# Kernel tuning notes

Measured on AMD Instinct MI355X. Metric: run time of the kernel, lower is better.

## Reference

```python
import jax, jax.numpy as jnp
import numpy as np

N_HEADS = 16

def setup_inputs() -> dict:
    key = jax.random.key(0)
    ks = jax.random.split(key, 5)
    b, t, k = 2, 2048, 1024
    x = jax.random.normal(ks[0], (b, t, k), dtype=jnp.float32)
    Wq = jax.random.normal(ks[1], (k, k), dtype=jnp.float32) * 0.02
    Wk = jax.random.normal(ks[2], (k, k), dtype=jnp.float32) * 0.02
    Wv = jax.random.normal(ks[3], (k, k), dtype=jnp.float32) * 0.02
    Wo = jax.random.normal(ks[4], (k, k), dtype=jnp.float32) * 0.02
    return {"x": x, "Wq": Wq, "Wk": Wk, "Wv": Wv, "Wo": Wo}

def reference(x, Wq, Wk, Wv, Wo):
    b, t, k = x.shape
    h = N_HEADS
    hs = k // h
    # torch nn.Linear(k, k, bias=False): y = x @ W.T
    Q = (x @ Wq.T).reshape(b, t, h, hs).transpose(0, 2, 1, 3)  # [b,h,t,hs]
    K = (x @ Wk.T).reshape(b, t, h, hs).transpose(0, 2, 1, 3)
    V = (x @ Wv.T).reshape(b, t, h, hs).transpose(0, 2, 1, 3)
    # NOTE: original scales by 1/sqrt(k) (full model dim), not 1/sqrt(hs)
    scores = jnp.einsum('bhqd,bhkd->bhqk', Q, K) / jnp.sqrt(jnp.float32(k))
    causal = jnp.tril(jnp.ones((t, t), dtype=bool))  # [t,t]
    scores = jnp.where(causal[None, None], scores, jnp.float32(-jnp.inf))
    P = jax.nn.softmax(scores, axis=-1)  # [b,h,t,t]
    O = jnp.einsum('bhqk,bhkd->bhqd', P, V)  # [b,h,t,hs]
    O = O.transpose(0, 2, 1, 3).reshape(b, t, k)
    return O @ Wo.T
```

## Files before the change

### kernel.cpp

```cpp
#include <hip/hip_runtime.h>
#include <hip/hip_bf16.h>

typedef __attribute__((ext_vector_type(8))) short bf16x8;
typedef __attribute__((ext_vector_type(4))) float f32x4;
typedef unsigned short u16;
typedef unsigned int u32;

#define MFMA16(a, b, c) __builtin_amdgcn_mfma_f32_16x16x32_bf16((a), (b), (c), 0, 0, 0)

__device__ __forceinline__ void gld16(const void* g, void* l) {
  __builtin_amdgcn_global_load_lds((const __attribute__((address_space(1))) u32*)g,
                                   (__attribute__((address_space(3))) u32*)l, 16, 0, 0);
}

__device__ __forceinline__ u16 f2bf(float f) {
  u32 x = __float_as_uint(f);
  x += 0x7fffu + ((x >> 16) & 1u);
  return (u16)(x >> 16);
}
__device__ __forceinline__ u32 pk2(float lo, float hi) {
  return (u32)f2bf(lo) | ((u32)f2bf(hi) << 16);
}
__device__ __forceinline__ u32 cvtpk(float lo, float hi) {
  u32 r;
  asm("v_cvt_pk_bf16_f32 %0, %1, %2" : "=v"(r) : "v"(lo), "v"(hi));
  return r;
}
__device__ __forceinline__ bf16x8 ldfrag(const u16* lds, int row, int kbyte) {
  return *(const bf16x8*)&lds[row * 64 + ((kbyte ^ ((row & 7) << 4)) >> 1)];
}

__global__ __launch_bounds__(256) void cvt_bf16(const float* __restrict__ s, u16* __restrict__ d,
                                                int n4) {
  int i = blockIdx.x * 256 + threadIdx.x;
  if (i < n4) {
    float4 f = ((const float4*)s)[i];
    uint2 o;
    o.x = pk2(f.x, f.y);
    o.y = pk2(f.z, f.w);
    ((uint2*)d)[i] = o;
  }
}

__global__ __launch_bounds__(256) void cvt_w4(const float* __restrict__ w0,
                                              const float* __restrict__ w1,
                                              const float* __restrict__ w2,
                                              const float* __restrict__ w3,
                                              u16* __restrict__ d012, u16* __restrict__ d3) {
  const int y = blockIdx.y;
  const float* s = (y == 0) ? w0 : (y == 1) ? w1 : (y == 2) ? w2 : w3;
  u16* d = (y == 3) ? d3 : d012 + (size_t)y * 1024 * 1024;
  int i = blockIdx.x * 256 + threadIdx.x;
  float4 f = ((const float4*)s)[i];
  uint2 o;
  o.x = pk2(f.x, f.y);
  o.y = pk2(f.z, f.w);
  ((uint2*)d)[i] = o;
}

template <int MODE, bool BBF, int BM>
__global__ __launch_bounds__(256) void gemm2(const u16* __restrict__ Ab,
                                             const float* __restrict__ W0,
                                             const float* __restrict__ W1,
                                             const float* __restrict__ W2,
                                             const u16* __restrict__ Bb, u16* __restrict__ Cq,
                                             u16* __restrict__ Ck, u16* __restrict__ Cvt,
                                             float* __restrict__ Cf) {
  constexpr int MI = BM / 32;
  __shared__ u16 Alds[BM * 64];
  __shared__ u16 Blds[128 * 64];
  const int tid = threadIdx.x, wid = tid >> 6, lane = tid & 63;
  const int lg = lane >> 4, lr = lane & 15;
  const int wr = wid >> 1, wc = wid & 1;
  const int bm = blockIdx.y, bn = blockIdx.x;
  const int ng = bn * 128;

  const float* Bf = nullptr;
  const u16* Bbr = nullptr;
  if constexpr (BBF) {
    Bbr = Bb + (size_t)ng * 1024;
  } else {
    if constexpr (MODE == 0)
      Bf = (ng < 1024 ? W0 : (ng < 2048 ? W1 : W2)) + (size_t)(ng & 1023) * 1024;
    else
      Bf = W0 + (size_t)ng * 1024;
  }

  f32x4 acc[MI][4];
#pragma unroll
  for (int i = 0; i < MI; ++i)
#pragma unroll
    for (int j = 0; j < 4; ++j) acc[i][j] = {0.f, 0.f, 0.f, 0.f};

  const u16* Ag0 = Ab + (size_t)(bm * BM) * 1024;
  const int srow8 = lane >> 3, schunk = lane & 7;
  const int brow = tid >> 1, bhalf = tid & 1;

  for (int kt = 0; kt < 16; ++kt) {
    __syncthreads();
#pragma unroll
    for (int c = 0; c < BM / 32; ++c) {
      int rb = (c * 4 + wid) * 8;
      int row = rb + srow8;
      int ch = schunk ^ srow8;
      gld16(Ag0 + (size_t)row * 1024 + kt * 64 + ch * 8, (void*)&Alds[rb * 64]);
    }
    if constexpr (BBF) {
#pragma unroll
      for (int c = 0; c < 4; ++c) {
        int rb = (c * 4 + wid) * 8;
        int row = rb + srow8;
        int ch = schunk ^ srow8;
        gld16(Bbr + (size_t)row * 1024 + kt * 64 + ch * 8, (void*)&Blds[rb * 64]);
      }
    } else {
      const float* s = Bf + (size_t)brow * 1024 + kt * 64 + bhalf * 32;
#pragma unroll
      for (int q = 0; q < 4; ++q) {
        float4 f0 = ((const float4*)s)[2 * q];
        float4 f1 = ((const float4*)s)[2 * q + 1];
        uint4 w;
        w.x = pk2(f0.x, f0.y);
        w.y = pk2(f0.z, f0.w);
        w.z = pk2(f1.x, f1.y);
        w.w = pk2(f1.z, f1.w);
        int ch = (bhalf * 4 + q) ^ (brow & 7);
        *(uint4*)&Blds[brow * 64 + ch * 8] = w;
      }
    }
    __syncthreads();

#pragma unroll
    for (int ks = 0; ks < 2; ++ks) {
      bf16x8 af[MI], bfr[4];
#pragma unroll
      for (int mi = 0; mi < MI; ++mi)
        af[mi] = ldfrag(Alds, wr * (BM / 2) + mi * 16 + lr, ks * 64 + lg * 16);
#pragma unroll
      for (int ni = 0; ni < 4; ++ni) bfr[ni] = ldfrag(Blds, wc * 64 + ni * 16 + lr, ks * 64 + lg * 16);
#pragma unroll
      for (int mi = 0; mi < MI; ++mi)
#pragma unroll
        for (int ni = 0; ni < 4; ++ni) acc[mi][ni] = MFMA16(af[mi], bfr[ni], acc[mi][ni]);
    }
  }

  if constexpr (MODE == 1) {
#pragma unroll
    for (int mi = 0; mi < MI; ++mi)
#pragma unroll
      for (int r = 0; r < 4; ++r) {
        int m = bm * BM + wr * (BM / 2) + mi * 16 + lg * 4 + r;
#pragma unroll
        for (int ni = 0; ni < 4; ++ni)
          Cf[(size_t)m * 1024 + ng + wc * 64 + ni * 16 + lr] = acc[mi][ni][r];
      }
  } else if (ng < 2048) {
    u16* C = (ng < 1024) ? Cq : Ck;
    const float qs = (ng < 1024) ? 0.0450842200f : 1.0f;
    const int nb = ng & 1023;
#pragma unroll
    for (int mi = 0; mi < MI; ++mi)
#pragma unroll
      for (int r = 0; r < 4; ++r) {
        int m = bm * BM + wr * (BM / 2) + mi * 16 + lg * 4 + r;
#pragma unroll
        for (int ni = 0; ni < 4; ++ni)
          C[(size_t)m * 1024 + nb + wc * 64 + ni * 16 + lr] = f2bf(acc[mi][ni][r] * qs);
      }
  } else {
    const int bnum = (bm * BM) >> 11;
    const int nvb = (ng - 2048) + wc * 64;
#pragma unroll
    for (int mi = 0; mi < MI; ++mi) {
      int tb = ((bm * BM) & 2047) + wr * (BM / 2) + mi * 16 + lg * 4;
#pragma unroll
      for (int ni = 0; ni < 4; ++ni) {
        int nv = nvb + ni * 16 + lr;
        ushort4 st;
        st.x = f2bf(acc[mi][ni][0]);
        st.y = f2bf(acc[mi][ni][1]);
        st.z = f2bf(acc[mi][ni][2]);
        st.w = f2bf(acc[mi][ni][3]);
        *(ushort4*)&Cvt[((size_t)(bnum << 10) + nv) * 2048 + tb] = st;
      }
    }
  }
}

__global__ __launch_bounds__(256, 4) void flash6(const u16* __restrict__ Qb,
                                                 const u16* __restrict__ Kb,
                                                 const u16* __restrict__ Vt,
                                                 u16* __restrict__ Ob) {
  __shared__ u16 Klds[2][64 * 64];
  __shared__ u16 Vlds[2][64 * 64];
  __shared__ u16 Plds[4][16 * 64];
  const int tid = threadIdx.x, wid = tid >> 6, lane = tid & 63;
  const int lg = lane >> 4, lr = lane & 15;
  const int bid = blockIdx.x;
  const int xcd = bid & 7;
  const int slot = bid >> 3;
  const int cp = slot & 31;
  const int g = slot >> 5;
  const int hb = xcd * 4 + g;
  const int hh = hb & 15, bb = hb >> 4;
  const int m0 = (cp + ((g >> 1) << 3)) & 31;
  const int base = (m0 & 1) ? (m0 >> 1) : (31 - (m0 >> 1));
  const int jq = (g & 1) ? (31 - base) : base;
  const int q0 = jq * 64;
  const size_t baseqk = ((size_t)bb * 2048) * 1024 + hh * 64;
  const u16* Vth = Vt + ((size_t)(bb * 1024 + hh * 64)) * 2048;
  const int srow8 = lane >> 3, schunk = lane & 7;

  bf16x8 qf[2];
  {
    const u16* qp = Qb + baseqk + (size_t)(q0 + wid * 16 + lr) * 1024 + lg * 8;
    qf[0] = *(const bf16x8*)qp;
    qf[1] = *(const bf16x8*)(qp + 32);
  }
  f32x4 acc[4];
#pragma unroll
  for (int dt = 0; dt < 4; ++dt) acc[dt] = {0.f, 0.f, 0.f, 0.f};
  float l_r = 0.f;
  const int qrow = q0 + wid * 16 + lr;

  auto stage = [&](int buf, int kv0) {
#pragma unroll
    for (int c2 = 0; c2 < 2; ++c2) {
      int rb = (c2 * 4 + wid) * 8;
      int row = rb + srow8;
      int ch = schunk ^ srow8;
      gld16(Kb + baseqk + (size_t)(kv0 + row) * 1024 + ch * 8, (void*)&Klds[buf][rb * 64]);
      gld16(Vth + (size_t)row * 2048 + kv0 + ch * 8, (void*)&Vlds[buf][rb * 64]);
    }
  };

  const int ntiles = jq + 1;
  stage(0, 0);
  __syncthreads();

  u16* Pw = &Plds[wid][0];
  const int pswz = (lr & 7) << 3;

  for (int t = 0; t < ntiles; ++t) {
    const int cur = t & 1;
    if (t + 1 < ntiles) stage(cur ^ 1, (t + 1) * 64);
    const int kv0 = t * 64;
    const u16* Kl = &Klds[cur][0];
    const u16* Vl = &Vlds[cur][0];

    f32x4 s[4];
#pragma unroll
    for (int ni = 0; ni < 4; ++ni) s[ni] = {0.f, 0.f, 0.f, 0.f};
    __builtin_amdgcn_s_setprio(1);
#pragma unroll
    for (int ks = 0; ks < 2; ++ks) {
#pragma unroll
      for (int ni = 0; ni < 4; ++ni) {
        bf16x8 kb = ldfrag(Kl, ni * 16 + lr, ks * 64 + lg * 16);
        s[ni] = MFMA16(kb, qf[ks], s[ni]);
      }
    }
    __builtin_amdgcn_s_setprio(0);

    float p[4][4];
    float rs = 0.f;
    if (t == jq) {
#pragma unroll
      for (int ni = 0; ni < 4; ++ni)
#pragma unroll
        for (int r = 0; r < 4; ++r) {
          float v = s[ni][r];
          if (kv0 + ni * 16 + lg * 4 + r > qrow) v = -1e30f;
          v = exp2f(v);
          p[ni][r] = v;
          rs += v;
        }
    } else {
#pragma unroll
      for (int ni = 0; ni < 4; ++ni)
#pragma unroll
        for (int r = 0; r < 4; ++r) {
          float v = exp2f(s[ni][r]);
          p[ni][r] = v;
          rs += v;
        }
    }
    l_r += rs;

#pragma unroll
    for (int ni = 0; ni < 4; ++ni) {
#pragma unroll
      for (int h = 0; h < 2; ++h) {
        u32 w = cvtpk(p[ni][2 * h], p[ni][2 * h + 1]);
        int col = (ni * 16 + lg * 4 + 2 * h) ^ pswz;
        *(u32*)&Pw[lr * 64 + col] = w;
      }
    }
    bf16x8 pb0 = *(const bf16x8*)&Pw[lr * 64 + ((lg * 8) ^ pswz)];
    bf16x8 pb1 = *(const bf16x8*)&Pw[lr * 64 + ((32 + lg * 8) ^ pswz)];
    __builtin_amdgcn_s_setprio(1);
#pragma unroll
    for (int dt = 0; dt < 4; ++dt) {
      bf16x8 a0 = ldfrag(Vl, dt * 16 + lr, lg * 16);
      bf16x8 a1 = ldfrag(Vl, dt * 16 + lr, 64 + lg * 16);
      acc[dt] = MFMA16(a0, pb0, acc[dt]);
      acc[dt] = MFMA16(a1, pb1, acc[dt]);
    }
    __builtin_amdgcn_s_setprio(0);
    __syncthreads();
  }

  l_r += __shfl_xor(l_r, 16);
  l_r += __shfl_xor(l_r, 32);

  {
    float inv = 1.f / l_r;
    u16* orow = Ob + baseqk + (size_t)qrow * 1024 + lg * 4;
#pragma unroll
    for (int dt = 0; dt < 4; ++dt) {
      ushort4 st;
      st.x = f2bf(acc[dt][0] * inv);
      st.y = f2bf(acc[dt][1] * inv);
      st.z = f2bf(acc[dt][2] * inv);
      st.w = f2bf(acc[dt][3] * inv);
      *(ushort4*)&orow[dt * 16] = st;
    }
  }
}

extern "C" void kernel_launch(void* const* d_in, const int* in_sizes, int n_in, void* d_out,
                              int out_size, void* d_ws, size_t ws_size, hipStream_t stream) {
  const float* x = (const float*)d_in[0];
  const float* Wq = (const float*)d_in[1];
  const float* Wk = (const float*)d_in[2];
  const float* Wv = (const float*)d_in[3];
  const float* Wo = (const float*)d_in[4];
  float* out = (float*)d_out;

  u16* xb = (u16*)d_ws;
  u16* Qb = xb + (size_t)4096 * 1024;
  u16* Kb = Qb + (size_t)4096 * 1024;
  u16* Vt = Kb + (size_t)4096 * 1024;
  u16* Ob = Qb;
  u16* Wb = Vt + (size_t)4096 * 1024;
  u16* Wob = Wb + (size_t)3072 * 1024;

  const bool full = ws_size >= ((size_t)40 << 20);

  cvt_bf16<<<4096, 256, 0, stream>>>(x, xb, 4096 * 1024 / 4);
  if (full) {
    cvt_w4<<<dim3(1024, 4), 256, 0, stream>>>(Wq, Wk, Wv, Wo, Wb, Wob);
    gemm2<0, true, 128><<<dim3(24, 32), 256, 0, stream>>>(xb, nullptr, nullptr, nullptr, Wb, Qb,
                                                          Kb, Vt, nullptr);
    flash6<<<1024, 256, 0, stream>>>(Qb, Kb, Vt, Ob);
    gemm2<1, true, 64><<<dim3(8, 64), 256, 0, stream>>>(Ob, nullptr, nullptr, nullptr, Wob,
                                                        nullptr, nullptr, nullptr, out);
  } else {
    gemm2<0, false, 128><<<dim3(24, 32), 256, 0, stream>>>(xb, Wq, Wk, Wv, nullptr, Qb, Kb, Vt,
                                                           nullptr);
    flash6<<<1024, 256, 0, stream>>>(Qb, Kb, Vt, Ob);
    gemm2<1, false, 64><<<dim3(8, 64), 256, 0, stream>>>(Ob, Wo, nullptr, nullptr, nullptr,
                                                         nullptr, nullptr, nullptr, out);
  }
}
```

Before: 116.2 us.

## Split long causal attention rows across two kernels with partial accumulators

The flash attention kernel now caps every query block at 16 KV tiles. Query blocks past index 16 write unnormalised bf16 partial accumulators and row sums to workspace. A second kernel with 512 blocks reloads those partials and processes the remaining KV tiles before normalising, which splits the longest causal rows across two launches to even out load. In exchange it adds an extra launch, partial round-trips through global memory with bf16 rounding of the accumulators, and a serial dependency. It also reuses the xb buffer as scratch.

```diff
diff --git a/kernel.cpp b/kernel.cpp
--- a/kernel.cpp
+++ b/kernel.cpp
@@ -188,10 +188,11 @@
   }
 }
 
-__global__ __launch_bounds__(256, 4) void flash6(const u16* __restrict__ Qb,
+__global__ __launch_bounds__(256, 4) void flashA(const u16* __restrict__ Qb,
                                                  const u16* __restrict__ Kb,
                                                  const u16* __restrict__ Vt,
-                                                 u16* __restrict__ Ob) {
+                                                 u16* __restrict__ Ob, u16* __restrict__ accP,
+                                                 float* __restrict__ lP) {
   __shared__ u16 Klds[2][64 * 64];
   __shared__ u16 Vlds[2][64 * 64];
   __shared__ u16 Plds[4][16 * 64];
@@ -200,13 +201,14 @@
   const int bid = blockIdx.x;
   const int xcd = bid & 7;
   const int slot = bid >> 3;
-  const int cp = slot & 31;
-  const int g = slot >> 5;
+  const int cp = slot & 31, g = slot >> 5;
   const int hb = xcd * 4 + g;
   const int hh = hb & 15, bb = hb >> 4;
   const int m0 = (cp + ((g >> 1) << 3)) & 31;
-  const int base = (m0 & 1) ? (m0 >> 1) : (31 - (m0 >> 1));
-  const int jq = (g & 1) ? (31 - base) : base;
+  const int basej = (m0 & 1) ? (m0 >> 1) : (31 - (m0 >> 1));
+  const int jq = (g & 1) ? (31 - basej) : basej;
+  const bool split = jq >= 16;
+  const int t1 = split ? 16 : jq + 1;
   const int q0 = jq * 64;
   const size_t baseqk = ((size_t)bb * 2048) * 1024 + hh * 64;
   const u16* Vth = Vt + ((size_t)(bb * 1024 + hh * 64)) * 2048;
@@ -235,16 +237,15 @@
     }
   };
 
-  const int ntiles = jq + 1;
   stage(0, 0);
   __syncthreads();
 
   u16* Pw = &Plds[wid][0];
   const int pswz = (lr & 7) << 3;
 
-  for (int t = 0; t < ntiles; ++t) {
+  for (int t = 0; t < t1; ++t) {
     const int cur = t & 1;
-    if (t + 1 < ntiles) stage(cur ^ 1, (t + 1) * 64);
+    if (t + 1 < t1) stage(cur ^ 1, (t + 1) * 64);
     const int kv0 = t * 64;
     const u16* Kl = &Klds[cur][0];
     const u16* Vl = &Vlds[cur][0];
@@ -265,7 +266,7 @@
 
     float p[4][4];
     float rs = 0.f;
-    if (t == jq) {
+    if (!split && t == jq) {
 #pragma unroll
       for (int ni = 0; ni < 4; ++ni)
 #pragma unroll
@@ -311,8 +312,175 @@
     __syncthreads();
   }
 
+  if (split) {
+    const int pidx = hb * 16 + (jq - 16);
+    u16* pp = accP + ((size_t)(pidx * 64 + wid * 16 + lr)) * 64 + lg * 4;
+#pragma unroll
+    for (int dt = 0; dt < 4; ++dt) {
+      ushort4 st;
+      st.x = f2bf(acc[dt][0]);
+      st.y = f2bf(acc[dt][1]);
+      st.z = f2bf(acc[dt][2]);
+      st.w = f2bf(acc[dt][3]);
+      *(ushort4*)&pp[dt * 16] = st;
+    }
+    l_r += __shfl_xor(l_r, 16);
+    l_r += __shfl_xor(l_r, 32);
+    if (lg == 0) lP[pidx * 64 + wid * 16 + lr] = l_r;
+  } else {
+    l_r += __shfl_xor(l_r, 16);
+    l_r += __shfl_xor(l_r, 32);
+    float inv = 1.f / l_r;
+    u16* orow = Ob + baseqk + (size_t)qrow * 1024 + lg * 4;
+#pragma unroll
+    for (int dt = 0; dt < 4; ++dt) {
+      ushort4 st;
+      st.x = f2bf(acc[dt][0] * inv);
+      st.y = f2bf(acc[dt][1] * inv);
+      st.z = f2bf(acc[dt][2] * inv);
+      st.w = f2bf(acc[dt][3] * inv);
+      *(ushort4*)&orow[dt * 16] = st;
+    }
+  }
+}
+
+__global__ __launch_bounds__(256, 4) void flashB(const u16* __restrict__ Qb,
+                                                 const u16* __restrict__ Kb,
+                                                 const u16* __restrict__ Vt,
+                                                 u16* __restrict__ Ob,
+                                                 const u16* __restrict__ accP,
+                                                 const float* __restrict__ lP) {
+  __shared__ u16 Klds[2][64 * 64];
+  __shared__ u16 Vlds[2][64 * 64];
+  __shared__ u16 Plds[4][16 * 64];
+  const int tid = threadIdx.x, wid = tid >> 6, lane = tid & 63;
+  const int lg = lane >> 4, lr = lane & 15;
+  const int bid = blockIdx.x;
+  const int xcd = bid & 7;
+  const int slot = bid >> 3;
+  const int cp = slot & 15, g = slot >> 4;
+  const int hb = xcd * 4 + g;
+  const int hh = hb & 15, bb = hb >> 4;
+  const int m0 = (cp + ((g >> 1) << 3)) & 15;
+  const int basej = (m0 & 1) ? (m0 >> 1) : (15 - (m0 >> 1));
+  const int jq = 16 + ((g & 1) ? (15 - basej) : basej);
+  const int pidx = hb * 16 + (jq - 16);
+  const int q0 = jq * 64;
+  const size_t baseqk = ((size_t)bb * 2048) * 1024 + hh * 64;
+  const u16* Vth = Vt + ((size_t)(bb * 1024 + hh * 64)) * 2048;
+  const int srow8 = lane >> 3, schunk = lane & 7;
+
+  bf16x8 qf[2];
+  {
+    const u16* qp = Qb + baseqk + (size_t)(q0 + wid * 16 + lr) * 1024 + lg * 8;
+    qf[0] = *(const bf16x8*)qp;
+    qf[1] = *(const bf16x8*)(qp + 32);
+  }
+  const int qrow = q0 + wid * 16 + lr;
+
+  auto stage = [&](int buf, int kv0) {
+#pragma unroll
+    for (int c2 = 0; c2 < 2; ++c2) {
+      int rb = (c2 * 4 + wid) * 8;
+      int row = rb + srow8;
+      int ch = schunk ^ srow8;
+      gld16(Kb + baseqk + (size_t)(kv0 + row) * 1024 + ch * 8, (void*)&Klds[buf][rb * 64]);
+      gld16(Vth + (size_t)row * 2048 + kv0 + ch * 8, (void*)&Vlds[buf][rb * 64]);
+    }
+  };
+
+  stage(0, 16 * 64);
+
+  f32x4 acc[4];
+  {
+    const u16* pp = accP + ((size_t)(pidx * 64 + wid * 16 + lr)) * 64 + lg * 4;
+#pragma unroll
+    for (int dt = 0; dt < 4; ++dt) {
+      ushort4 pv = *(const ushort4*)&pp[dt * 16];
+      acc[dt][0] = __uint_as_float((u32)pv.x << 16);
+      acc[dt][1] = __uint_as_float((u32)pv.y << 16);
+      acc[dt][2] = __uint_as_float((u32)pv.z << 16);
+      acc[dt][3] = __uint_as_float((u32)pv.w << 16);
+    }
+  }
+  float l_r = 0.f;
+  __syncthreads();
+
+  u16* Pw = &Plds[wid][0];
+  const int pswz = (lr & 7) << 3;
+
+  for (int t = 16; t <= jq; ++t) {
+    const int cur = t & 1;
+    if (t < jq) stage(cur ^ 1, (t + 1) * 64);
+    const int kv0 = t * 64;
+    const u16* Kl = &Klds[cur][0];
+    const u16* Vl = &Vlds[cur][0];
+
+    f32x4 s[4];
+#pragma unroll
+    for (int ni = 0; ni < 4; ++ni) s[ni] = {0.f, 0.f, 0.f, 0.f};
+    __builtin_amdgcn_s_setprio(1);
+#pragma unroll
+    for (int ks = 0; ks < 2; ++ks) {
+#pragma unroll
+      for (int ni = 0; ni < 4; ++ni) {
+        bf16x8 kb = ldfrag(Kl, ni * 16 + lr, ks * 64 + lg * 16);
+        s[ni] = MFMA16(kb, qf[ks], s[ni]);
+      }
+    }
+    __builtin_amdgcn_s_setprio(0);
+
+    float p[4][4];
+    float rs = 0.f;
+    if (t == jq) {
+#pragma unroll
+      for (int ni = 0; ni < 4; ++ni)
+#pragma unroll
+        for (int r = 0; r < 4; ++r) {
+          float v = s[ni][r];
+          if (kv0 + ni * 16 + lg * 4 + r > qrow) v = -1e30f;
+          v = exp2f(v);
+          p[ni][r] = v;
+          rs += v;
+        }
+    } else {
+#pragma unroll
+      for (int ni = 0; ni < 4; ++ni)
+#pragma unroll
+        for (int r = 0; r < 4; ++r) {
+          float v = exp2f(s[ni][r]);
+          p[ni][r] = v;
+          rs += v;
+        }
+    }
+    l_r += rs;
+
+#pragma unroll
+    for (int ni = 0; ni < 4; ++ni) {
+#pragma unroll
+      for (int h = 0; h < 2; ++h) {
+        u32 w = cvtpk(p[ni][2 * h], p[ni][2 * h + 1]);
+        int col = (ni * 16 + lg * 4 + 2 * h) ^ pswz;
+        *(u32*)&Pw[lr * 64 + col] = w;
+      }
+    }
+    bf16x8 pb0 = *(const bf16x8*)&Pw[lr * 64 + ((lg * 8) ^ pswz)];
+    bf16x8 pb1 = *(const bf16x8*)&Pw[lr * 64 + ((32 + lg * 8) ^ pswz)];
+    __builtin_amdgcn_s_setprio(1);
+#pragma unroll
+    for (int dt = 0; dt < 4; ++dt) {
+      bf16x8 a0 = ldfrag(Vl, dt * 16 + lr, lg * 16);
+      bf16x8 a1 = ldfrag(Vl, dt * 16 + lr, 64 + lg * 16);
+      acc[dt] = MFMA16(a0, pb0, acc[dt]);
+      acc[dt] = MFMA16(a1, pb1, acc[dt]);
+    }
+    __builtin_amdgcn_s_setprio(0);
+    __syncthreads();
+  }
+
   l_r += __shfl_xor(l_r, 16);
   l_r += __shfl_xor(l_r, 32);
+  l_r += lP[pidx * 64 + wid * 16 + lr];
 
   {
     float inv = 1.f / l_r;
@@ -345,6 +513,8 @@
   u16* Ob = Qb;
   u16* Wb = Vt + (size_t)4096 * 1024;
   u16* Wob = Wb + (size_t)3072 * 1024;
+  u16* accP = xb;
+  float* lP = (float*)(xb + (size_t)512 * 64 * 64);
 
   const bool full = ws_size >= ((size_t)40 << 20);
 
@@ -353,13 +523,15 @@
     cvt_w4<<<dim3(1024, 4), 256, 0, stream>>>(Wq, Wk, Wv, Wo, Wb, Wob);
     gemm2<0, true, 128><<<dim3(24, 32), 256, 0, stream>>>(xb, nullptr, nullptr, nullptr, Wb, Qb,
                                                           Kb, Vt, nullptr);
-    flash6<<<1024, 256, 0, stream>>>(Qb, Kb, Vt, Ob);
+    flashA<<<1024, 256, 0, stream>>>(Qb, Kb, Vt, Ob, accP, lP);
+    flashB<<<512, 256, 0, stream>>>(Qb, Kb, Vt, Ob, accP, lP);
     gemm2<1, true, 64><<<dim3(8, 64), 256, 0, stream>>>(Ob, nullptr, nullptr, nullptr, Wob,
                                                         nullptr, nullptr, nullptr, out);
   } else {
     gemm2<0, false, 128><<<dim3(24, 32), 256, 0, stream>>>(xb, Wq, Wk, Wv, nullptr, Qb, Kb, Vt,
                                                            nullptr);
-    flash6<<<1024, 256, 0, stream>>>(Qb, Kb, Vt, Ob);
+    flashA<<<1024, 256, 0, stream>>>(Qb, Kb, Vt, Ob, accP, lP);
+    flashB<<<512, 256, 0, stream>>>(Qb, Kb, Vt, Ob, accP, lP);
     gemm2<1, false, 64><<<dim3(8, 64), 256, 0, stream>>>(Ob, Wo, nullptr, nullptr, nullptr,
                                                          nullptr, nullptr, nullptr, out);
   }
```

New measurement: 127.7 us. 1.1x slower.

## Split long causal query tiles across KV halves with a combine kernel

Applied to the files above, without the earlier changes.

Query tiles in the upper half of the causal range are split into two KV-range halves, processed by separate blocks that write unnormalized bf16 partial accumulators and row sums. A new combine kernel adds the partials and normalizes into the output. This balances per-block work to about 16 KV tiles and raises the block count so the causal tail is shorter. It adds a kernel launch, extra global memory traffic for partials, and bf16 rounding of partial accumulators.

```diff
diff --git a/kernel.cpp b/kernel.cpp
--- a/kernel.cpp
+++ b/kernel.cpp
@@ -188,10 +188,11 @@
   }
 }
 
-__global__ __launch_bounds__(256, 4) void flash6(const u16* __restrict__ Qb,
+__global__ __launch_bounds__(256, 4) void flashC(const u16* __restrict__ Qb,
                                                  const u16* __restrict__ Kb,
                                                  const u16* __restrict__ Vt,
-                                                 u16* __restrict__ Ob) {
+                                                 u16* __restrict__ Ob, u16* __restrict__ accP,
+                                                 float* __restrict__ lP) {
   __shared__ u16 Klds[2][64 * 64];
   __shared__ u16 Vlds[2][64 * 64];
   __shared__ u16 Plds[4][16 * 64];
@@ -200,14 +201,25 @@
   const int bid = blockIdx.x;
   const int xcd = bid & 7;
   const int slot = bid >> 3;
-  const int cp = slot & 31;
-  const int g = slot >> 5;
+  int g, jq;
+  bool typeY;
+  if (slot < 64) {
+    g = slot >> 4;
+    jq = 16 + (slot & 15);
+    typeY = false;
+  } else {
+    int idx = slot - 64;
+    int len = 16 - (idx >> 3);
+    int j = idx & 7;
+    g = j & 3;
+    typeY = (j >> 2) != 0;
+    jq = typeY ? (15 + len) : (len - 1);
+  }
   const int hb = xcd * 4 + g;
   const int hh = hb & 15, bb = hb >> 4;
-  const int m0 = (cp + ((g >> 1) << 3)) & 31;
-  const int base = (m0 & 1) ? (m0 >> 1) : (31 - (m0 >> 1));
-  const int jq = (g & 1) ? (31 - base) : base;
   const int q0 = jq * 64;
+  const int t0 = typeY ? 16 : 0;
+  const int t1 = (!typeY && jq >= 16) ? 16 : (jq + 1);
   const size_t baseqk = ((size_t)bb * 2048) * 1024 + hh * 64;
   const u16* Vth = Vt + ((size_t)(bb * 1024 + hh * 64)) * 2048;
   const int srow8 = lane >> 3, schunk = lane & 7;
@@ -235,16 +247,15 @@
     }
   };
 
-  const int ntiles = jq + 1;
-  stage(0, 0);
+  stage(0, t0 * 64);
   __syncthreads();
 
   u16* Pw = &Plds[wid][0];
   const int pswz = (lr & 7) << 3;
 
-  for (int t = 0; t < ntiles; ++t) {
+  for (int t = t0; t < t1; ++t) {
     const int cur = t & 1;
-    if (t + 1 < ntiles) stage(cur ^ 1, (t + 1) * 64);
+    if (t + 1 < t1) stage(cur ^ 1, (t + 1) * 64);
     const int kv0 = t * 64;
     const u16* Kl = &Klds[cur][0];
     const u16* Vl = &Vlds[cur][0];
@@ -311,10 +322,9 @@
     __syncthreads();
   }
 
-  l_r += __shfl_xor(l_r, 16);
-  l_r += __shfl_xor(l_r, 32);
-
-  {
+  if (!typeY && jq < 16) {
+    l_r += __shfl_xor(l_r, 16);
+    l_r += __shfl_xor(l_r, 32);
     float inv = 1.f / l_r;
     u16* orow = Ob + baseqk + (size_t)qrow * 1024 + lg * 4;
 #pragma unroll
@@ -326,7 +336,47 @@
       st.w = f2bf(acc[dt][3] * inv);
       *(ushort4*)&orow[dt * 16] = st;
     }
-  }
+  } else {
+    const int p = (typeY ? 512 : 0) + hb * 16 + (jq - 16);
+    u16* pp = accP + (size_t)p * 4096 + (size_t)(wid * 16 + lr) * 64 + lg * 4;
+#pragma unroll
+    for (int dt = 0; dt < 4; ++dt) {
+      ushort4 st;
+      st.x = f2bf(acc[dt][0]);
+      st.y = f2bf(acc[dt][1]);
+      st.z = f2bf(acc[dt][2]);
+      st.w = f2bf(acc[dt][3]);
+      *(ushort4*)&pp[dt * 16] = st;
+    }
+    l_r += __shfl_xor(l_r, 16);
+    l_r += __shfl_xor(l_r, 32);
+    if (lg == 0) lP[p * 64 + wid * 16 + lr] = l_r;
+  }
+}
+
+__global__ __launch_bounds__(256) void fcomb(const u16* __restrict__ accP,
+                                             const float* __restrict__ lP,
+                                             u16* __restrict__ Ob) {
+  const int pid = blockIdx.x, tid = threadIdx.x;
+  const int hb = pid >> 4, jq = 16 + (pid & 15);
+  const int bb = hb >> 4, hh = hb & 15;
+  const int row = tid >> 2, dseg = (tid & 3) << 4;
+  const u16* a0 = accP + (size_t)pid * 4096 + row * 64 + dseg;
+  const u16* a1 = accP + (size_t)(pid + 512) * 4096 + row * 64 + dseg;
+  float inv = 1.f / (lP[pid * 64 + row] + lP[(pid + 512) * 64 + row]);
+  u16 b0[16], b1[16], ov[16];
+  *(uint4*)&b0[0] = ((const uint4*)a0)[0];
+  *(uint4*)&b0[8] = ((const uint4*)a0)[1];
+  *(uint4*)&b1[0] = ((const uint4*)a1)[0];
+  *(uint4*)&b1[8] = ((const uint4*)a1)[1];
+#pragma unroll
+  for (int i = 0; i < 16; ++i) {
+    float f = __uint_as_float((u32)b0[i] << 16) + __uint_as_float((u32)b1[i] << 16);
+    ov[i] = f2bf(f * inv);
+  }
+  u16* od = Ob + (size_t)bb * 2048 * 1024 + (size_t)(jq * 64 + row) * 1024 + hh * 64 + dseg;
+  ((uint4*)od)[0] = *(uint4*)&ov[0];
+  ((uint4*)od)[1] = *(uint4*)&ov[8];
 }
 
 extern "C" void kernel_launch(void* const* d_in, const int* in_sizes, int n_in, void* d_out,
@@ -345,21 +395,25 @@
   u16* Ob = Qb;
   u16* Wb = Vt + (size_t)4096 * 1024;
   u16* Wob = Wb + (size_t)3072 * 1024;
+  u16* accP = xb;
 
   const bool full = ws_size >= ((size_t)40 << 20);
+  float* lP = full ? (float*)Wb : (float*)(Vt + (size_t)4096 * 1024);
 
   cvt_bf16<<<4096, 256, 0, stream>>>(x, xb, 4096 * 1024 / 4);
   if (full) {
     cvt_w4<<<dim3(1024, 4), 256, 0, stream>>>(Wq, Wk, Wv, Wo, Wb, Wob);
     gemm2<0, true, 128><<<dim3(24, 32), 256, 0, stream>>>(xb, nullptr, nullptr, nullptr, Wb, Qb,
                                                           Kb, Vt, nullptr);
-    flash6<<<1024, 256, 0, stream>>>(Qb, Kb, Vt, Ob);
+    flashC<<<1536, 256, 0, stream>>>(Qb, Kb, Vt, Ob, accP, lP);
+    fcomb<<<512, 256, 0, stream>>>(accP, lP, Ob);
     gemm2<1, true, 64><<<dim3(8, 64), 256, 0, stream>>>(Ob, nullptr, nullptr, nullptr, Wob,
                                                         nullptr, nullptr, nullptr, out);
   } else {
     gemm2<0, false, 128><<<dim3(24, 32), 256, 0, stream>>>(xb, Wq, Wk, Wv, nullptr, Qb, Kb, Vt,
                                                            nullptr);
-    flash6<<<1024, 256, 0, stream>>>(Qb, Kb, Vt, Ob);
+    flashC<<<1536, 256, 0, stream>>>(Qb, Kb, Vt, Ob, accP, lP);
+    fcomb<<<512, 256, 0, stream>>>(accP, lP, Ob);
     gemm2<1, false, 64><<<dim3(8, 64), 256, 0, stream>>>(Ob, Wo, nullptr, nullptr, nullptr,
                                                          nullptr, nullptr, nullptr, out);
   }
```

Result: no change. 116.2 us (-0.0%).
